# Kernel tuning notes

Measured on AMD Instinct MI355X. Metric: run time of the kernel, lower is better.

Reference implementation:

```python
import jax, jax.numpy as jnp
import numpy as np

B, C, W, H = 2, 64, 96, 96  # N = W*H = 9216 spatial positions


def conv1x1(x, w, b):
    # x: (B, Cin, W, H), w: (Cout, Cin), b: (Cout,) -> (B, Cout, W, H)
    return jnp.einsum('bchw,oc->bohw', x, w) + b[None, :, None, None]


def setup_inputs() -> dict:
    key = jax.random.key(0)
    ks = jax.random.split(key, 4)
    c8 = C // 8
    s = 0.05  # small weight scale keeps softmax logits in a sane range
    return {
        'x': jax.random.normal(ks[0], (B, C, W, H), jnp.float32),
        'wq': jax.random.normal(ks[1], (c8, C), jnp.float32) * s,
        'bq': jnp.zeros((c8,), jnp.float32),
        'wk': jax.random.normal(ks[2], (c8, C), jnp.float32) * s,
        'bk': jnp.zeros((c8,), jnp.float32),
        'wv': jax.random.normal(ks[3], (C, C), jnp.float32) * s,
        'bv': jnp.zeros((C,), jnp.float32),
        'gamma': jnp.full((1,), 0.5, jnp.float32),
    }


def reference(x, wq, bq, wk, bk, wv, bv, gamma):
    b, c, w, h = x.shape
    n = w * h
    q = conv1x1(x, wq, bq).reshape(b, -1, n)   # (B, C//8, N)
    k = conv1x1(x, wk, bk).reshape(b, -1, n)   # (B, C//8, N)
    v = conv1x1(x, wv, bv).reshape(b, c, n)    # (B, C, N)
    energy = jnp.einsum('bci,bcj->bij', q, k)  # (B, N, N)
    attn = jax.nn.softmax(energy, axis=-1)
    # torch.bmm(v, attn): out[b,c,i] = sum_j v[b,c,j] * attn[b,j,i]
    out = jnp.einsum('bcj,bji->bci', v, attn).reshape(b, c, w, h)
    return gamma * out + x
```

## Files before the change

### kernel.cpp

```cpp
#include <hip/hip_runtime.h>

using half2v  = __attribute__((ext_vector_type(2))) _Float16;
using half4   = __attribute__((ext_vector_type(4))) _Float16;
using half8   = __attribute__((ext_vector_type(8))) _Float16;
using floatx4 = __attribute__((ext_vector_type(4))) float;

constexpr int BATCH = 2;
constexpr int NPOS  = 96 * 96;
constexpr int NT    = NPOS / 16;
constexpr int NST   = NPOS / 32;

#define EXP2(x) __builtin_amdgcn_exp2f(x)
#define MFMA16(A, B, C) __builtin_amdgcn_mfma_f32_16x16x16f16(A, B, C, 0, 0, 0)
#define MFMA32(A, B, C) __builtin_amdgcn_mfma_f32_16x16x32_f16(A, B, C, 0, 0, 0)

__device__ inline half8 p8_of(floatx4 e0, floatx4 e1) {
    half2v a0 = __builtin_bit_cast(half2v,
        __builtin_amdgcn_cvt_pkrtz(EXP2(e0[0]), EXP2(e0[1])));
    half2v a1 = __builtin_bit_cast(half2v,
        __builtin_amdgcn_cvt_pkrtz(EXP2(e0[2]), EXP2(e0[3])));
    half2v a2 = __builtin_bit_cast(half2v,
        __builtin_amdgcn_cvt_pkrtz(EXP2(e1[0]), EXP2(e1[1])));
    half2v a3 = __builtin_bit_cast(half2v,
        __builtin_amdgcn_cvt_pkrtz(EXP2(e1[2]), EXP2(e1[3])));
    half8 p = {a0[0], a0[1], a1[0], a1[1], a2[0], a2[1], a3[0], a3[1]};
    return p;
}

__global__ __launch_bounds__(256) void qkv_kernel(
    const float* __restrict__ x,
    const float* __restrict__ wq, const float* __restrict__ bq,
    const float* __restrict__ wk, const float* __restrict__ bk,
    const float* __restrict__ wv, const float* __restrict__ bv,
    _Float16* __restrict__ Qf, _Float16* __restrict__ Kf,
    _Float16* __restrict__ Vf)
{
    __shared__ float W[80][64];
    __shared__ float bias[80];
    __shared__ float qs[32][9];
    __shared__ float ks[32][9];
    __shared__ _Float16 vs[32][72];
    const int tid = threadIdx.x;
    for (int idx = tid; idx < 80 * 64; idx += 256) {
        int o = idx >> 6, c = idx & 63;
        float w;
        if (o < 8)       w = wq[o * 64 + c];
        else if (o < 16) w = wk[(o - 8) * 64 + c];
        else             w = wv[(o - 16) * 64 + c];
        W[o][c] = w;
    }
    if (tid < 80) {
        float bb;
        if (tid < 8)       bb = bq[tid];
        else if (tid < 16) bb = bk[tid - 8];
        else               bb = bv[tid - 16];
        bias[tid] = bb;
    }
    __syncthreads();

    const int js = blockIdx.x;
    const int b  = blockIdx.y;
    const int part = tid >> 5;
    const int jl   = tid & 31;
    const int i    = js * 32 + jl;

    float xr[64];
    #pragma unroll
    for (int c = 0; c < 64; ++c)
        xr[c] = x[(size_t)(b * 64 + c) * NPOS + i];

    #pragma unroll
    for (int q = 0; q < 10; ++q) {
        const int o = part * 10 + q;
        float s = bias[o];
        #pragma unroll
        for (int c4 = 0; c4 < 16; ++c4) {
            float4 w4 = *(const float4*)&W[o][c4 * 4];
            s += w4.x * xr[c4*4+0] + w4.y * xr[c4*4+1]
               + w4.z * xr[c4*4+2] + w4.w * xr[c4*4+3];
        }
        if (o < 8)       qs[jl][o] = s;
        else if (o < 16) ks[jl][o - 8] = s;
        else             vs[jl][o - 16] = (_Float16)s;
    }
    __syncthreads();

    const size_t tile = (size_t)b * NST + js;
    {
        const int ct = tid >> 6, l = tid & 63;
        const int g = l >> 4, cl = l & 15;
        half8 o8;
        #pragma unroll
        for (int idx = 0; idx < 8; ++idx)
            o8[idx] = vs[8 * g + idx][16 * ct + cl];
        *(half8*)&Vf[(tile * 256 + ct * 64 + l) * 8] = o8;
    }
    if (tid < 128) {
        const int l = tid >> 1, e = tid & 1;
        const int m = l & 15, g = l >> 4;
        const int jsrc = 8 * (m >> 2) + 4 * e + (m & 3);
        constexpr float LOG2E = 1.44269504088896f;
        half4 qh;
        #pragma unroll
        for (int r = 0; r < 4; ++r)
            qh[r] = (g < 2) ? (_Float16)(qs[jsrc][4 * g + r] * LOG2E)
                            : (_Float16)0.f;
        ((half4*)Qf)[(tile * 64 + l) * 2 + e] = qh;
    } else {
        const int t = tid - 128;
        const int ht = t >> 6, l = t & 63;
        const int il = l & 15, g = l >> 4;
        const int it = js * 2 + ht;
        half4 kh;
        #pragma unroll
        for (int r = 0; r < 4; ++r) {
            if (g < 2)       kh[r] = (_Float16)ks[16 * ht + il][4 * g + r];
            else if (g == 2) kh[r] = (r < 2) ? (_Float16)1.f : (_Float16)0.f;
            else             kh[r] = (_Float16)0.f;
        }
        ((half4*)Kf)[(size_t)(b * NT + it) * 64 + l] = kh;
    }
}

__global__ __launch_bounds__(256, 4) void denom_kernel(
    _Float16* __restrict__ Qf, const _Float16* __restrict__ Kf)
{
    __shared__ float LpS[4][32];
    const int tid = threadIdx.x;
    const int w = tid >> 6, l = tid & 63;
    const int js = blockIdx.x;
    const int b  = blockIdx.y;
    const size_t tile = (size_t)b * NST + js;
    const half8* __restrict__ qfb = (const half8*)Qf + (size_t)b * NST * 64;
    const half4* __restrict__ kfb = (const half4*)Kf + (size_t)b * NT * 64;

    half8 qv = qfb[tile % ((size_t)NST) * 64 + ((size_t)0) + js * 0 + (size_t)js * 64 - (size_t)js * 64 + (size_t)js * 64 + l];
    qv = qfb[(size_t)js * 64 + l];
    half4 q0 = __builtin_shufflevector(qv, qv, 0, 1, 2, 3);
    half4 q1 = __builtin_shufflevector(qv, qv, 4, 5, 6, 7);

    float sum[2][4];
    #pragma unroll
    for (int e = 0; e < 2; ++e)
        #pragma unroll
        for (int r = 0; r < 4; ++r) sum[e][r] = 0.f;

    const floatx4 z = {0.f, 0.f, 0.f, 0.f};
    #define DACC(E0, E1) do { \
        _Pragma("unroll") \
        for (int r = 0; r < 4; ++r) { \
            sum[0][r] += EXP2(E0[r]); sum[1][r] += EXP2(E1[r]); } \
    } while (0)

    const half4* kp = kfb + (size_t)w * 64 + l;
    half4 kfA = kp[0];
    half4 kfB = kp[256];
    floatx4 eA0 = MFMA16(q0, kfA, z), eA1 = MFMA16(q1, kfA, z);
    floatx4 eB0, eB1;
    for (int k = 0; k < 71; ++k) {
        kfA = kp[(size_t)(2 * k + 2) * 256];
        eB0 = MFMA16(q0, kfB, z); eB1 = MFMA16(q1, kfB, z);
        DACC(eA0, eA1);
        kfB = kp[(size_t)(2 * k + 3) * 256];
        eA0 = MFMA16(q0, kfA, z); eA1 = MFMA16(q1, kfA, z);
        DACC(eB0, eB1);
    }
    eB0 = MFMA16(q0, kfB, z); eB1 = MFMA16(q1, kfB, z);
    DACC(eA0, eA1);
    DACC(eB0, eB1);
    #undef DACC

    #pragma unroll
    for (int e = 0; e < 2; ++e)
        #pragma unroll
        for (int r = 0; r < 4; ++r)
            #pragma unroll
            for (int m = 1; m < 16; m <<= 1)
                sum[e][r] += __shfl_xor(sum[e][r], m, 64);

    if ((l & 15) == 0) {
        const int g = l >> 4;
        #pragma unroll
        for (int e = 0; e < 2; ++e)
            #pragma unroll
            for (int r = 0; r < 4; ++r)
                LpS[w][8 * g + 4 * e + r] = sum[e][r];
    }
    __syncthreads();

    if (tid < 32) {
        const float L = LpS[0][tid] + LpS[1][tid] + LpS[2][tid] + LpS[3][tid];
        const float v = -__log2f(L);
        _Float16 hi = (_Float16)v;
        _Float16 lo = (_Float16)(v - (float)hi);
        const int m = 4 * (tid >> 3) + (tid & 3);
        const int e = (tid >> 2) & 1;
        half2v hl = {hi, lo};
        ((half2v*)Qf)[((tile * 64 + m + 32) * 2 + e) * 2] = hl;
    }
}

__global__ __launch_bounds__(256, 3) void attn_kernel(
    const _Float16* __restrict__ Qf, const _Float16* __restrict__ Kf,
    const _Float16* __restrict__ Vf,
    const float* __restrict__ x, const float* __restrict__ gamma,
    float* __restrict__ out)
{
    __shared__ float red[4][3][64][9];
    const int s = blockIdx.x;
    const int xcd = s & 7;
    const int b   = xcd >> 2;
    const int r2  = (s >> 3) * 4 + (xcd & 3);
    const int igl = r2 % 192;
    const int ch  = r2 / 192;
    const int tid = threadIdx.x;
    const int w = tid >> 6, l = tid & 63;
    const int it0 = igl * 3, i0 = igl * 48;

    const half8* __restrict__ qfb = (const half8*)Qf + (size_t)b * NST * 64;
    const half4* __restrict__ kfb = (const half4*)Kf + (size_t)b * NT * 64;
    const half8* __restrict__ vfb = (const half8*)Vf + (size_t)b * NST * 256;

    half4 kf[3];
    #pragma unroll
    for (int st = 0; st < 3; ++st) kf[st] = kfb[(size_t)(it0 + st) * 64 + l];

    floatx4 acc[3][2];
    #pragma unroll
    for (int st = 0; st < 3; ++st) {
        acc[st][0] = (floatx4){0.f, 0.f, 0.f, 0.f};
        acc[st][1] = (floatx4){0.f, 0.f, 0.f, 0.f};
    }

    const floatx4 z = {0.f, 0.f, 0.f, 0.f};

    #define E_STEP(QV, E) do { \
        half4 qe0 = __builtin_shufflevector(QV, QV, 0, 1, 2, 3); \
        half4 qe1 = __builtin_shufflevector(QV, QV, 4, 5, 6, 7); \
        E[0] = MFMA16(qe0, kf[0], z); E[1] = MFMA16(qe1, kf[0], z); \
        E[2] = MFMA16(qe0, kf[1], z); E[3] = MFMA16(qe1, kf[1], z); \
        E[4] = MFMA16(qe0, kf[2], z); E[5] = MFMA16(qe1, kf[2], z); \
    } while (0)

    #define PXV(E, V0, V1) do { \
        half8 p0 = p8_of(E[0], E[1]); \
        half8 p1 = p8_of(E[2], E[3]); \
        half8 p2 = p8_of(E[4], E[5]); \
        acc[0][0] = MFMA32(V0, p0, acc[0][0]); \
        acc[0][1] = MFMA32(V1, p0, acc[0][1]); \
        acc[1][0] = MFMA32(V0, p1, acc[1][0]); \
        acc[1][1] = MFMA32(V1, p1, acc[1][1]); \
        acc[2][0] = MFMA32(V0, p2, acc[2][0]); \
        acc[2][1] = MFMA32(V1, p2, acc[2][1]); \
    } while (0)

    const half8* qpw = qfb + (size_t)w * 64 + l;
    const half8* vpw = vfb + (size_t)w * 256 + ch * 128 + l;

    floatx4 eA[6], eB[6];
    half8 qvA = qpw[0];
    half8 v0A = vpw[0],    v1A = vpw[64];
    half8 qvB = qpw[256];
    half8 v0B = vpw[1024], v1B = vpw[1024 + 64];
    E_STEP(qvA, eA);

    for (int k = 0; k < 35; ++k) {
        const size_t s2 = (size_t)(2 * k + 2), s3 = (size_t)(2 * k + 3);
        qvA = qpw[s2 * 256];
        E_STEP(qvB, eB);
        PXV(eA, v0A, v1A);
        v0A = vpw[s2 * 1024]; v1A = vpw[s2 * 1024 + 64];
        qvB = qpw[s3 * 256];
        E_STEP(qvA, eA);
        PXV(eB, v0B, v1B);
        v0B = vpw[s3 * 1024]; v1B = vpw[s3 * 1024 + 64];
    }
    E_STEP(qvB, eB);
    PXV(eA, v0A, v1A);
    PXV(eB, v0B, v1B);
    #undef E_STEP
    #undef PXV

    #pragma unroll
    for (int st = 0; st < 3; ++st)
        #pragma unroll
        for (int t2 = 0; t2 < 2; ++t2)
            #pragma unroll
            for (int r = 0; r < 4; ++r)
                red[w][st][l][t2 * 4 + r] = acc[st][t2][r];
    __syncthreads();

    if (w < 3) {
        const float g = gamma[0];
        const int iq = i0 + 16 * w + (l & 15);
        #pragma unroll
        for (int t2 = 0; t2 < 2; ++t2)
            #pragma unroll
            for (int r = 0; r < 4; ++r) {
                float v = red[0][w][l][t2*4+r] + red[1][w][l][t2*4+r]
                        + red[2][w][l][t2*4+r] + red[3][w][l][t2*4+r];
                int c = 16 * (2 * ch + t2) + 4 * (l >> 4) + r;
                size_t o = ((size_t)(b * 64 + c)) * NPOS + iq;
                out[o] = g * v + x[o];
            }
    }
}

extern "C" void kernel_launch(void* const* d_in, const int* in_sizes, int n_in,
                              void* d_out, int out_size, void* d_ws, size_t ws_size,
                              hipStream_t stream)
{
    const float* x     = (const float*)d_in[0];
    const float* wq    = (const float*)d_in[1];
    const float* bq    = (const float*)d_in[2];
    const float* wk    = (const float*)d_in[3];
    const float* bk    = (const float*)d_in[4];
    const float* wv    = (const float*)d_in[5];
    const float* bv    = (const float*)d_in[6];
    const float* gamma = (const float*)d_in[7];
    float* out = (float*)d_out;

    char* wsb = (char*)d_ws;
    _Float16* Qf = (_Float16*)wsb;
    _Float16* Kf = (_Float16*)(wsb + 589824);
    _Float16* Vf = (_Float16*)(wsb + 1179648);

    qkv_kernel<<<dim3(NST, BATCH), 256, 0, stream>>>(
        x, wq, bq, wk, bk, wv, bv, Qf, Kf, Vf);

    denom_kernel<<<dim3(NST, BATCH), 256, 0, stream>>>(Qf, Kf);

    attn_kernel<<<dim3(768), 256, 0, stream>>>(Qf, Kf, Vf, x, gamma, out);
}
```

Measured before the change: 144.8 us.

## Compute all 64 output channels per attention block, halving energy recomputation

Each attention block now covers all 64 value channels instead of splitting them into two halves across blocks. The energy/exp computation for each query-key tile is therefore done once rather than twice, and the grid shrinks from 768 to 384 blocks. The loop is restructured into a single-stage software pipeline that prefetches the next Q/V fragments, with the exp and PV MFMAs interleaved per sub-tile. The cost is more accumulator registers and a larger shared reduction buffer, with launch bounds lowered from 3 to 2 blocks per SM, so occupancy and latency hiding may drop.

```diff
diff --git a/kernel.cpp b/kernel.cpp
--- a/kernel.cpp
+++ b/kernel.cpp
@@ -134,8 +134,7 @@
     const half8* __restrict__ qfb = (const half8*)Qf + (size_t)b * NST * 64;
     const half4* __restrict__ kfb = (const half4*)Kf + (size_t)b * NT * 64;
 
-    half8 qv = qfb[tile % ((size_t)NST) * 64 + ((size_t)0) + js * 0 + (size_t)js * 64 - (size_t)js * 64 + (size_t)js * 64 + l];
-    qv = qfb[(size_t)js * 64 + l];
+    half8 qv = qfb[(size_t)js * 64 + l];
     half4 q0 = __builtin_shufflevector(qv, qv, 0, 1, 2, 3);
     half4 q1 = __builtin_shufflevector(qv, qv, 4, 5, 6, 7);
 
@@ -200,19 +199,16 @@
     }
 }
 
-__global__ __launch_bounds__(256, 3) void attn_kernel(
+__global__ __launch_bounds__(256, 2) void attn_kernel(
     const _Float16* __restrict__ Qf, const _Float16* __restrict__ Kf,
     const _Float16* __restrict__ Vf,
     const float* __restrict__ x, const float* __restrict__ gamma,
     float* __restrict__ out)
 {
-    __shared__ float red[4][3][64][9];
+    __shared__ float red[4][3][64][17];
     const int s = blockIdx.x;
-    const int xcd = s & 7;
-    const int b   = xcd >> 2;
-    const int r2  = (s >> 3) * 4 + (xcd & 3);
-    const int igl = r2 % 192;
-    const int ch  = r2 / 192;
+    const int b   = s & 1;
+    const int igl = s >> 1;
     const int tid = threadIdx.x;
     const int w = tid >> 6, l = tid & 63;
     const int it0 = igl * 3, i0 = igl * 48;
@@ -225,81 +221,65 @@
     #pragma unroll
     for (int st = 0; st < 3; ++st) kf[st] = kfb[(size_t)(it0 + st) * 64 + l];
 
-    floatx4 acc[3][2];
-    #pragma unroll
-    for (int st = 0; st < 3; ++st) {
-        acc[st][0] = (floatx4){0.f, 0.f, 0.f, 0.f};
-        acc[st][1] = (floatx4){0.f, 0.f, 0.f, 0.f};
-    }
+    floatx4 acc[3][4];
+    #pragma unroll
+    for (int st = 0; st < 3; ++st)
+        #pragma unroll
+        for (int ct = 0; ct < 4; ++ct)
+            acc[st][ct] = (floatx4){0.f, 0.f, 0.f, 0.f};
 
     const floatx4 z = {0.f, 0.f, 0.f, 0.f};
 
-    #define E_STEP(QV, E) do { \
+    #define ASTEP(QV, V0, V1, V2, V3) do { \
         half4 qe0 = __builtin_shufflevector(QV, QV, 0, 1, 2, 3); \
         half4 qe1 = __builtin_shufflevector(QV, QV, 4, 5, 6, 7); \
-        E[0] = MFMA16(qe0, kf[0], z); E[1] = MFMA16(qe1, kf[0], z); \
-        E[2] = MFMA16(qe0, kf[1], z); E[3] = MFMA16(qe1, kf[1], z); \
-        E[4] = MFMA16(qe0, kf[2], z); E[5] = MFMA16(qe1, kf[2], z); \
+        _Pragma("unroll") \
+        for (int st = 0; st < 3; ++st) { \
+            floatx4 e0 = MFMA16(qe0, kf[st], z); \
+            floatx4 e1 = MFMA16(qe1, kf[st], z); \
+            half8 p = p8_of(e0, e1); \
+            acc[st][0] = MFMA32(V0, p, acc[st][0]); \
+            acc[st][1] = MFMA32(V1, p, acc[st][1]); \
+            acc[st][2] = MFMA32(V2, p, acc[st][2]); \
+            acc[st][3] = MFMA32(V3, p, acc[st][3]); \
+        } \
     } while (0)
 
-    #define PXV(E, V0, V1) do { \
-        half8 p0 = p8_of(E[0], E[1]); \
-        half8 p1 = p8_of(E[2], E[3]); \
-        half8 p2 = p8_of(E[4], E[5]); \
-        acc[0][0] = MFMA32(V0, p0, acc[0][0]); \
-        acc[0][1] = MFMA32(V1, p0, acc[0][1]); \
-        acc[1][0] = MFMA32(V0, p1, acc[1][0]); \
-        acc[1][1] = MFMA32(V1, p1, acc[1][1]); \
-        acc[2][0] = MFMA32(V0, p2, acc[2][0]); \
-        acc[2][1] = MFMA32(V1, p2, acc[2][1]); \
-    } while (0)
-
     const half8* qpw = qfb + (size_t)w * 64 + l;
-    const half8* vpw = vfb + (size_t)w * 256 + ch * 128 + l;
-
-    floatx4 eA[6], eB[6];
-    half8 qvA = qpw[0];
-    half8 v0A = vpw[0],    v1A = vpw[64];
-    half8 qvB = qpw[256];
-    half8 v0B = vpw[1024], v1B = vpw[1024 + 64];
-    E_STEP(qvA, eA);
-
-    for (int k = 0; k < 35; ++k) {
-        const size_t s2 = (size_t)(2 * k + 2), s3 = (size_t)(2 * k + 3);
-        qvA = qpw[s2 * 256];
-        E_STEP(qvB, eB);
-        PXV(eA, v0A, v1A);
-        v0A = vpw[s2 * 1024]; v1A = vpw[s2 * 1024 + 64];
-        qvB = qpw[s3 * 256];
-        E_STEP(qvA, eA);
-        PXV(eB, v0B, v1B);
-        v0B = vpw[s3 * 1024]; v1B = vpw[s3 * 1024 + 64];
-    }
-    E_STEP(qvB, eB);
-    PXV(eA, v0A, v1A);
-    PXV(eB, v0B, v1B);
-    #undef E_STEP
-    #undef PXV
+    const half8* vpw = vfb + (size_t)w * 256 + l;
+
+    half8 qv = qpw[0];
+    half8 v0 = vpw[0], v1 = vpw[64], v2 = vpw[128], v3 = vpw[192];
+    for (int k = 0; k < 71; ++k) {
+        const size_t nx = (size_t)(k + 1);
+        half8 qn  = qpw[nx * 256];
+        half8 v0n = vpw[nx * 1024],       v1n = vpw[nx * 1024 + 64];
+        half8 v2n = vpw[nx * 1024 + 128], v3n = vpw[nx * 1024 + 192];
+        ASTEP(qv, v0, v1, v2, v3);
+        qv = qn; v0 = v0n; v1 = v1n; v2 = v2n; v3 = v3n;
+    }
+    ASTEP(qv, v0, v1, v2, v3);
+    #undef ASTEP
 
     #pragma unroll
     for (int st = 0; st < 3; ++st)
         #pragma unroll
-        for (int t2 = 0; t2 < 2; ++t2)
+        for (int ct = 0; ct < 4; ++ct)
             #pragma unroll
             for (int r = 0; r < 4; ++r)
-                red[w][st][l][t2 * 4 + r] = acc[st][t2][r];
+                red[w][st][l][ct * 4 + r] = acc[st][ct][r];
     __syncthreads();
 
     if (w < 3) {
         const float g = gamma[0];
         const int iq = i0 + 16 * w + (l & 15);
         #pragma unroll
-        for (int t2 = 0; t2 < 2; ++t2)
+        for (int ct = 0; ct < 4; ++ct)
             #pragma unroll
             for (int r = 0; r < 4; ++r) {
-                float v = red[0][w][l][t2*4+r] + red[1][w][l][t2*4+r]
-                        + red[2][w][l][t2*4+r] + red[3][w][l][t2*4+r];
-                int c = 16 * (2 * ch + t2) + 4 * (l >> 4) + r;
+                float v = red[0][w][l][ct*4+r] + red[1][w][l][ct*4+r]
+                        + red[2][w][l][ct*4+r] + red[3][w][l][ct*4+r];
+                int c = 16 * ct + 4 * (l >> 4) + r;
                 size_t o = ((size_t)(b * 64 + c)) * NPOS + iq;
                 out[o] = g * v + x[o];
             }
@@ -330,5 +310,5 @@
 
     denom_kernel<<<dim3(NST, BATCH), 256, 0, stream>>>(Qf, Kf);
 
-    attn_kernel<<<dim3(768), 256, 0, stream>>>(Qf, Kf, Vf, x, gamma, out);
-}
+    attn_kernel<<<dim3(384), 256, 0, stream>>>(Qf, Kf, Vf, x, gamma, out);
+}
```

After: 144.3 us. Within noise of the previous version (-0.3%).
